# Performance work log

Measured on AMD Instinct MI355X. Metric: run time of the kernel, lower is better.

## Reference

```python
import jax, jax.numpy as jnp
import numpy as np

NUM_HEADS = 8
EPS = 1e-6


def conv1x1(x, w, b):
    # x: [b,c,h,w], w: [out,in], b: [out]  (torch Conv2d 1x1 weight squeezed)
    return jnp.einsum('bchw,oc->bohw', x, w) + b[None, :, None, None]


def feature_map(x):
    return jax.nn.elu(x) + 1.0


def setup_inputs() -> dict:
    key = jax.random.key(0)
    ks = jax.random.split(key, 9)
    C = 512
    s = 1.0 / np.sqrt(C)
    x = jax.random.normal(ks[0], (8, C, 64, 64), dtype=jnp.float32)
    wq = jax.random.normal(ks[1], (C, C), dtype=jnp.float32) * s
    wk = jax.random.normal(ks[2], (C, C), dtype=jnp.float32) * s
    wv = jax.random.normal(ks[3], (C, C), dtype=jnp.float32) * s
    wo = jax.random.normal(ks[4], (C, C), dtype=jnp.float32) * s
    bq = jax.random.normal(ks[5], (C,), dtype=jnp.float32) * 0.01
    bk = jax.random.normal(ks[6], (C,), dtype=jnp.float32) * 0.01
    bv = jax.random.normal(ks[7], (C,), dtype=jnp.float32) * 0.01
    bo = jax.random.normal(ks[8], (C,), dtype=jnp.float32) * 0.01
    return {'x': x, 'wq': wq, 'bq': bq, 'wk': wk, 'bk': bk,
            'wv': wv, 'bv': bv, 'wo': wo, 'bo': bo}


def reference(x, wq, bq, wk, bk, wv, bv, wo, bo):
    b, c, h, w = x.shape
    nh = NUM_HEADS
    hd = c // nh
    L = h * w

    def to_heads(t):
        # [b,c,h,w] -> [b,nh,L,hd]
        return t.reshape(b, nh, hd, L).transpose(0, 1, 3, 2)

    Q = feature_map(to_heads(conv1x1(x, wq, bq)))
    K = feature_map(to_heads(conv1x1(x, wk, bk)))
    V = to_heads(conv1x1(x, wv, bv)) / L  # values / v_length

    KV = jnp.einsum('bhld,bhlv->bhdv', K, V)                 # [b,nh,hd,hd]
    Z = 1.0 / (jnp.einsum('bhld,bhd->bhl', Q, K.sum(axis=-2)) + EPS)
    out = jnp.einsum('bhld,bhdv,bhl->bhlv', Q, KV, Z) * L    # [b,nh,L,hd]

    out = out.transpose(0, 1, 3, 2).reshape(b, c, h, w)
    return conv1x1(out, wo, bo)
```

## Files before the change

### kernel.cpp

```cpp
#include <hip/hip_runtime.h>
#include <hip/hip_bf16.h>
#include <stdint.h>

#define BATCH 8
#define CCH   512
#define NHD   8
#define HD    64
#define LLEN  4096
#define M1    1536

typedef __bf16 bf16x8 __attribute__((ext_vector_type(8)));
typedef __bf16 bf16x4 __attribute__((ext_vector_type(4)));
typedef float  f32x4  __attribute__((ext_vector_type(4)));

__device__ __forceinline__ f32x4 mfma16(bf16x8 a, bf16x8 b, f32x4 c) {
  return __builtin_amdgcn_mfma_f32_16x16x32_bf16(a, b, c, 0, 0, 0);
}

__device__ __forceinline__ void gload_lds16(const void* g, void* l) {
  __builtin_amdgcn_global_load_lds(
      (const __attribute__((address_space(1))) uint32_t*)(uintptr_t)g,
      (__attribute__((address_space(3))) uint32_t*)(uintptr_t)l,
      16, 0, 0);
}

__global__ void pack_w(const float* __restrict__ wq, const float* __restrict__ wk,
                       const float* __restrict__ wv, const float* __restrict__ wo,
                       const float* __restrict__ bq, const float* __restrict__ bk,
                       const float* __restrict__ bv,
                       __bf16* __restrict__ wqkvb, __bf16* __restrict__ wob,
                       float* __restrict__ biasq) {
  const int n = M1 * CCH + CCH * CCH + M1;
  for (int i = blockIdx.x * blockDim.x + threadIdx.x; i < n; i += gridDim.x * blockDim.x) {
    if (i < M1 * CCH) {
      int r = i >> 9, c = i & 511;
      float v = (r < 512) ? wq[r * 512 + c]
              : (r < 1024) ? wk[(r - 512) * 512 + c]
                           : wv[(r - 1024) * 512 + c];
      wqkvb[i] = (__bf16)v;
    } else if (i < M1 * CCH + CCH * CCH) {
      int j = i - M1 * CCH;
      wob[j] = (__bf16)wo[j];
    } else {
      int j = i - M1 * CCH - CCH * CCH;
      biasq[j] = (j < 512) ? bq[j] : (j < 1024) ? bk[j - 512] : bv[j - 1024];
    }
  }
}

__global__ __launch_bounds__(256) void transpose_x(const float* __restrict__ x,
                                                   __bf16* __restrict__ xt) {
  __shared__ float tile[64][65];
  const int b = blockIdx.z, c0 = blockIdx.y * 64, l0 = blockIdx.x * 64;
  const int t = threadIdx.x;
  const int lq = (t & 15) * 4, cr = t >> 4;
  const float* xp = x + ((size_t)b * CCH + c0) * LLEN + l0;
#pragma unroll
  for (int q = 0; q < 4; ++q) {
    const int c = cr + q * 16;
    float4 v = *(const float4*)(xp + (size_t)c * LLEN + lq);
    tile[c][lq + 0] = v.x;
    tile[c][lq + 1] = v.y;
    tile[c][lq + 2] = v.z;
    tile[c][lq + 3] = v.w;
  }
  __syncthreads();
  __bf16* xo = xt + ((size_t)b * LLEN + l0) * CCH + c0;
  const int c4 = (t & 15) * 4, lr = t >> 4;
#pragma unroll
  for (int p = 0; p < 4; ++p) {
    const int l = lr + p * 16;
    bf16x4 o;
#pragma unroll
    for (int i = 0; i < 4; ++i) o[i] = (__bf16)tile[c4 + i][l];
    *(bf16x4*)(xo + (size_t)l * CCH + c4) = o;
  }
}

#define STAGE_A2(tt)                                                         \
  {                                                                          \
    const int bs = ((tt) & 3) * 16384;                                       \
    const int tK = (tt) * 32;                                                \
    gload_lds16(Ag + sOff + tK,         lds + bs + tid * 8);                 \
    gload_lds16(Ag + sOff + 65536 + tK, lds + bs + 4096 + tid * 8);          \
  }
#define STAGE_B2(tt)                                                         \
  {                                                                          \
    const int bs = ((tt) & 3) * 16384;                                       \
    const int tK = (tt) * 32;                                                \
    gload_lds16(Bg + sOff + tK,         lds + bs + 8192 + tid * 8);          \
    gload_lds16(Bg + sOff + 65536 + tK, lds + bs + 12288 + tid * 8);         \
  }

template <int EPI>
__global__ __launch_bounds__(512, 1) void gemm256(
    const __bf16* __restrict__ A, const __bf16* __restrict__ Bm,
    const float* __restrict__ bias,
    __bf16* __restrict__ qt, __bf16* __restrict__ kcm, __bf16* __restrict__ vcm,
    float* __restrict__ out) {
  __shared__ __attribute__((aligned(16))) __bf16 lds[4 * 16384];
  const int b  = blockIdx.z;
  const int n0 = blockIdx.x * 256;
  const int m0 = blockIdx.y * 256;
  const int tid = threadIdx.x;
  const int ll = tid & 63, w = tid >> 6;
  const int wr = w >> 2, wc = w & 3;
  const int lhi = ll >> 4, llo = ll & 15;

  const int Ra = wr * 128 + llo;
  const int aLane = ((Ra >> 1) << 6) + (((((Ra & 1) << 2) | lhi) ^ ((Ra >> 1) & 7)) << 3);
  const int Rb = wc * 64 + llo;
  const int bLane = 8192 + ((Rb >> 1) << 6) + (((((Rb & 1) << 2) | lhi) ^ ((Rb >> 1) & 7)) << 3);

  const int r2s = tid >> 3, c7u = (tid & 7) ^ (r2s & 7);
  const int sRow = (r2s << 1) | (c7u >> 2);
  const int sOff = sRow * CCH + ((c7u & 3) << 3);

  const __bf16* Ag = A + (size_t)m0 * CCH;
  const __bf16* Bg = Bm + ((size_t)b * LLEN + n0) * CCH;

  f32x4 acc[8][4] = {};

  STAGE_A2(0) STAGE_B2(0)
  STAGE_A2(1) STAGE_B2(1)
  asm volatile("s_waitcnt vmcnt(4)" ::: "memory");
  asm volatile("s_barrier" ::: "memory");

  for (int t = 0; t < 16; ++t) {
    const int cb = (t & 3) * 16384;
    bf16x8 af[4], bfr[4];
#pragma unroll
    for (int m = 0; m < 4; ++m) af[m] = *(const bf16x8*)(lds + cb + aLane + m * 512);
#pragma unroll
    for (int n = 0; n < 4; ++n) bfr[n] = *(const bf16x8*)(lds + cb + bLane + n * 512);
    if (t <= 13) STAGE_A2(t + 2)
    asm volatile("s_barrier" ::: "memory");
    asm volatile("s_waitcnt lgkmcnt(0)" ::: "memory");
    __builtin_amdgcn_sched_barrier(0);
    __builtin_amdgcn_s_setprio(1);
#pragma unroll
    for (int m = 0; m < 4; ++m)
#pragma unroll
      for (int n = 0; n < 4; ++n) acc[m][n] = mfma16(af[m], bfr[n], acc[m][n]);
    __builtin_amdgcn_s_setprio(0);
    asm volatile("s_barrier" ::: "memory");
#pragma unroll
    for (int m = 0; m < 4; ++m) af[m] = *(const bf16x8*)(lds + cb + aLane + (m + 4) * 512);
    if (t <= 13) STAGE_B2(t + 2)
    asm volatile("s_barrier" ::: "memory");
    asm volatile("s_waitcnt lgkmcnt(0)" ::: "memory");
    __builtin_amdgcn_sched_barrier(0);
    __builtin_amdgcn_s_setprio(1);
#pragma unroll
    for (int m = 0; m < 4; ++m)
#pragma unroll
      for (int n = 0; n < 4; ++n) acc[m + 4][n] = mfma16(af[m], bfr[n], acc[m + 4][n]);
    __builtin_amdgcn_s_setprio(0);
    if (t < 14)       asm volatile("s_waitcnt vmcnt(4)" ::: "memory");
    else if (t == 14) asm volatile("s_waitcnt vmcnt(0)" ::: "memory");
    asm volatile("s_barrier" ::: "memory");
  }

#pragma unroll
  for (int i = 0; i < 8; ++i) {
    const int o0 = m0 + wr * 128 + i * 16 + lhi * 4;
#pragma unroll
    for (int j = 0; j < 4; ++j) {
      const int col = n0 + wc * 64 + j * 16 + llo;
      if (EPI == 0) {
        if (m0 < 512) {
          bf16x4 pk;
#pragma unroll
          for (int r = 0; r < 4; ++r) {
            float tv = acc[i][j][r] + bias[o0 + r];
            tv = tv > 0.f ? tv + 1.f : __expf(tv);
            pk[r] = (__bf16)tv;
          }
          *(bf16x4*)(qt + ((size_t)b * LLEN + col) * CCH + o0) = pk;
        } else if (m0 < 1024) {
#pragma unroll
          for (int r = 0; r < 4; ++r) {
            float tv = acc[i][j][r] + bias[o0 + r];
            tv = tv > 0.f ? tv + 1.f : __expf(tv);
            kcm[((size_t)b * CCH + (o0 - 512 + r)) * LLEN + col] = (__bf16)tv;
          }
        } else {
#pragma unroll
          for (int r = 0; r < 4; ++r)
            vcm[((size_t)b * CCH + (o0 - 1024 + r)) * LLEN + col] =
                (__bf16)(acc[i][j][r] + bias[o0 + r]);
        }
      } else {
#pragma unroll
        for (int r = 0; r < 4; ++r)
          out[((size_t)b * CCH + o0 + r) * LLEN + col] = acc[i][j][r] + bias[o0 + r];
      }
    }
  }
}

__global__ __launch_bounds__(256) void kv_part_k(const __bf16* __restrict__ kcm,
                                                 const __bf16* __restrict__ vcm,
                                                 float* __restrict__ part,
                                                 float* __restrict__ part_ks) {
  __shared__ float red[8192];
  __shared__ float ksred[4][64];
  const int lc = blockIdx.x, bh = blockIdx.y;
  const int b = bh >> 3, h = bh & 7;
  const int tid = threadIdx.x;
  const int w = tid >> 6, ll = tid & 63, lhi = ll >> 4, llo = ll & 15;
  const __bf16* Kp = kcm + ((size_t)b * CCH + h * 64) * LLEN;
  const __bf16* Vp = vcm + ((size_t)b * CCH + h * 64) * LLEN;
  f32x4 acc[4][4];
#pragma unroll
  for (int i = 0; i < 4; ++i)
#pragma unroll
    for (int j = 0; j < 4; ++j) acc[i][j] = (f32x4){0.f, 0.f, 0.f, 0.f};
  float ks[4] = {0.f, 0.f, 0.f, 0.f};
  const int base = lc * 512 + w * 128 + lhi * 8;
#pragma unroll
  for (int kt = 0; kt < 4; ++kt) {
    const int k0 = base + kt * 32;
    bf16x8 af[4], bfr[4];
#pragma unroll
    for (int i = 0; i < 4; ++i) af[i]  = *(const bf16x8*)(Kp + (size_t)(i * 16 + llo) * LLEN + k0);
#pragma unroll
    for (int i = 0; i < 4; ++i) bfr[i] = *(const bf16x8*)(Vp + (size_t)(i * 16 + llo) * LLEN + k0);
#pragma unroll
    for (int i = 0; i < 4; ++i)
#pragma unroll
      for (int r = 0; r < 8; ++r) ks[i] += (float)af[i][r];
#pragma unroll
    for (int i = 0; i < 4; ++i)
#pragma unroll
      for (int j = 0; j < 4; ++j) acc[i][j] = mfma16(af[i], bfr[j], acc[i][j]);
  }
#pragma unroll
  for (int i = 0; i < 4; ++i) {
    float s = ks[i];
    s += __shfl_xor(s, 16);
    s += __shfl_xor(s, 32);
    if (lhi == 0) ksred[w][i * 16 + llo] = s;
  }
  if (w >= 2) {
#pragma unroll
    for (int i = 0; i < 4; ++i)
#pragma unroll
      for (int j = 0; j < 4; ++j)
        *(f32x4*)(red + (((w - 2) * 16 + i * 4 + j) << 8) + ll * 4) = acc[i][j];
  }
  __syncthreads();
  if (w < 2) {
#pragma unroll
    for (int i = 0; i < 4; ++i)
#pragma unroll
      for (int j = 0; j < 4; ++j)
        acc[i][j] += *(const f32x4*)(red + ((w * 16 + i * 4 + j) << 8) + ll * 4);
  }
  float ksv = 0.f;
  if (w == 1) ksv = ksred[0][ll] + ksred[1][ll] + ksred[2][ll] + ksred[3][ll];
  __syncthreads();
  if (w == 1) {
#pragma unroll
    for (int i = 0; i < 4; ++i)
#pragma unroll
      for (int j = 0; j < 4; ++j)
        *(f32x4*)(red + ((i * 4 + j) << 8) + ll * 4) = acc[i][j];
    part_ks[((size_t)lc * 64 + bh) * 64 + ll] = ksv;
  }
  __syncthreads();
  if (w == 0) {
    float* op = part + ((size_t)lc * 64 + bh) * 4096;
#pragma unroll
    for (int i = 0; i < 4; ++i)
#pragma unroll
      for (int j = 0; j < 4; ++j) {
        acc[i][j] += *(const f32x4*)(red + ((i * 4 + j) << 8) + ll * 4);
#pragma unroll
        for (int r = 0; r < 4; ++r) {
          int d = i * 16 + lhi * 4 + r, v = j * 16 + llo;
          op[d * 64 + v] = acc[i][j][r];
        }
      }
  }
}

__global__ void kv_red_k(const float* __restrict__ part, float* __restrict__ kv) {
  const int i = blockIdx.x * blockDim.x + threadIdx.x;
  float s = 0.f;
#pragma unroll
  for (int lc = 0; lc < 8; ++lc) s += part[(size_t)lc * 262144 + i];
  kv[i] = s;
}

__global__ void ksum_red_k(const float* __restrict__ part_ks, float* __restrict__ ksum) {
  const int i = blockIdx.x * blockDim.x + threadIdx.x;
  float s = 0.f;
#pragma unroll
  for (int lc = 0; lc < 8; ++lc) s += part_ks[(size_t)lc * 4096 + i];
  ksum[i] = s;
}

__global__ __launch_bounds__(256) void apply_k(const __bf16* __restrict__ qt,
                                               const float* __restrict__ kv,
                                               const float* __restrict__ ksum,
                                               __bf16* __restrict__ attn) {
  __shared__ __attribute__((aligned(16))) __bf16 kvT[64 * 68];
  __shared__ float zb[256];
  const int lc = blockIdx.x, bh = blockIdx.y;
  const int b = bh >> 3, h = bh & 7;
  const int tid = threadIdx.x;
  const float* kvp = kv + (size_t)bh * 4096;
  for (int i = tid; i < 4096; i += 256) {
    int d = i >> 6, v = i & 63;
    kvT[v * 68 + d] = (__bf16)kvp[i];
  }
  const int l = lc * 256 + tid;
  const __bf16* qp = qt + ((size_t)b * LLEN + l) * CCH + h * 64;
  const float* ksp = ksum + bh * 64;
  float s = 0.f;
#pragma unroll
  for (int d8 = 0; d8 < 64; d8 += 8) {
    bf16x8 qv = *(const bf16x8*)(qp + d8);
#pragma unroll
    for (int i = 0; i < 8; ++i) s += (float)qv[i] * ksp[d8 + i];
  }
  zb[tid] = 1.0f / (s + 1e-6f);
  __syncthreads();

  const int ll = tid & 63, w = tid >> 6, lhi = ll >> 4, llo = ll & 15;
  f32x4 acc[4][4];
#pragma unroll
  for (int i = 0; i < 4; ++i)
#pragma unroll
    for (int j = 0; j < 4; ++j) acc[i][j] = (f32x4){0.f, 0.f, 0.f, 0.f};
  const __bf16* qbase = qt + ((size_t)b * LLEN + lc * 256 + w * 64) * CCH + h * 64;
#pragma unroll
  for (int kt = 0; kt < 2; ++kt) {
    const int k8 = kt * 32 + lhi * 8;
    bf16x8 af[4], bfr[4];
#pragma unroll
    for (int i = 0; i < 4; ++i)
      af[i] = *(const bf16x8*)(qbase + (size_t)(i * 16 + llo) * CCH + k8);
#pragma unroll
    for (int j = 0; j < 4; ++j) {
      const __bf16* pb = kvT + (j * 16 + llo) * 68 + k8;
      ((bf16x4*)&bfr[j])[0] = *(const bf16x4*)pb;
      ((bf16x4*)&bfr[j])[1] = *(const bf16x4*)(pb + 4);
    }
#pragma unroll
    for (int i = 0; i < 4; ++i)
#pragma unroll
      for (int j = 0; j < 4; ++j) acc[i][j] = mfma16(af[i], bfr[j], acc[i][j]);
  }
  __bf16* ap = attn + ((size_t)b * LLEN + lc * 256) * CCH + h * 64;
#pragma unroll
  for (int i = 0; i < 4; ++i)
#pragma unroll
    for (int j = 0; j < 4; ++j)
#pragma unroll
      for (int r = 0; r < 4; ++r) {
        int ml = w * 64 + i * 16 + lhi * 4 + r;
        int v = j * 16 + llo;
        ap[(size_t)ml * CCH + v] = (__bf16)(acc[i][j][r] * zb[ml]);
      }
}

extern "C" void kernel_launch(void* const* d_in, const int* in_sizes, int n_in,
                              void* d_out, int out_size, void* d_ws, size_t ws_size,
                              hipStream_t stream) {
  const float* x  = (const float*)d_in[0];
  const float* wq = (const float*)d_in[1];
  const float* bq = (const float*)d_in[2];
  const float* wk = (const float*)d_in[3];
  const float* bk = (const float*)d_in[4];
  const float* wv = (const float*)d_in[5];
  const float* bv = (const float*)d_in[6];
  const float* wo = (const float*)d_in[7];
  const float* bo = (const float*)d_in[8];
  float* out = (float*)d_out;

  char* p = (char*)d_ws;
  __bf16* xt    = (__bf16*)p; p += (size_t)BATCH * LLEN * CCH * 2;
  __bf16* qt    = (__bf16*)p; p += (size_t)BATCH * LLEN * CCH * 2;
  __bf16* kcm   = (__bf16*)p; p += (size_t)BATCH * CCH * LLEN * 2;
  __bf16* vcm   = (__bf16*)p; p += (size_t)BATCH * CCH * LLEN * 2;
  __bf16* wqkvb = (__bf16*)p; p += (size_t)M1 * CCH * 2;
  __bf16* wob   = (__bf16*)p; p += (size_t)CCH * CCH * 2;
  float*  biasq = (float*)p;  p += (size_t)M1 * 4;
  float*  ksum  = (float*)p;  p += (size_t)BATCH * CCH * 4;
  float*  part  = (float*)p;  p += (size_t)8 * 64 * HD * HD * 4;
  float*  kvb   = (float*)p;  p += (size_t)64 * HD * HD * 4;
  float*  pks   = (float*)p;  p += (size_t)8 * 64 * 64 * 4;
  __bf16* attn  = xt;

  pack_w<<<1024, 256, 0, stream>>>(wq, wk, wv, wo, bq, bk, bv, wqkvb, wob, biasq);
  transpose_x<<<dim3(64, 8, BATCH), 256, 0, stream>>>(x, xt);
  gemm256<0><<<dim3(16, 6, BATCH), 512, 0, stream>>>(wqkvb, xt, biasq, qt, kcm, vcm, nullptr);
  kv_part_k<<<dim3(8, 64), 256, 0, stream>>>(kcm, vcm, part, pks);
  kv_red_k<<<1024, 256, 0, stream>>>(part, kvb);
  ksum_red_k<<<16, 256, 0, stream>>>(pks, ksum);
  apply_k<<<dim3(16, 64), 256, 0, stream>>>(qt, kvb, ksum, attn);
  gemm256<1><<<dim3(16, 2, BATCH), 512, 0, stream>>>(wob, attn, bo, nullptr, nullptr, nullptr, out);
}
```

Before: 176.1 us.

## Fold KV matrix into output projection weights and rework GEMM LDS layout

Replaces the per-token Q·KV apply kernel with a per-batch fold of Wo and KV into a combined weight, so the output GEMM consumes normalized Q directly. Q is scaled in place by the Z normalizer in a lightweight kernel. The GEMM's LDS swizzle and fragment loading are also reorganized, with a three-stage prefetch depth and loads of all eight A fragments per k-step. This is meant to remove the apply pass over Q and attention writes, at the cost of a per-batch 512x512 weight and batched A operands in the second GEMM.

```diff
diff --git a/kernel.cpp b/kernel.cpp
--- a/kernel.cpp
+++ b/kernel.cpp
@@ -25,12 +25,11 @@
 }
 
 __global__ void pack_w(const float* __restrict__ wq, const float* __restrict__ wk,
-                       const float* __restrict__ wv, const float* __restrict__ wo,
+                       const float* __restrict__ wv,
                        const float* __restrict__ bq, const float* __restrict__ bk,
                        const float* __restrict__ bv,
-                       __bf16* __restrict__ wqkvb, __bf16* __restrict__ wob,
-                       float* __restrict__ biasq) {
-  const int n = M1 * CCH + CCH * CCH + M1;
+                       __bf16* __restrict__ wqkvb, float* __restrict__ biasq) {
+  const int n = M1 * CCH + M1;
   for (int i = blockIdx.x * blockDim.x + threadIdx.x; i < n; i += gridDim.x * blockDim.x) {
     if (i < M1 * CCH) {
       int r = i >> 9, c = i & 511;
@@ -38,11 +37,8 @@
               : (r < 1024) ? wk[(r - 512) * 512 + c]
                            : wv[(r - 1024) * 512 + c];
       wqkvb[i] = (__bf16)v;
-    } else if (i < M1 * CCH + CCH * CCH) {
+    } else {
       int j = i - M1 * CCH;
-      wob[j] = (__bf16)wo[j];
-    } else {
-      int j = i - M1 * CCH - CCH * CCH;
       biasq[j] = (j < 512) ? bq[j] : (j < 1024) ? bk[j - 512] : bv[j - 1024];
     }
   }
@@ -77,19 +73,19 @@
   }
 }
 
-#define STAGE_A2(tt)                                                         \
-  {                                                                          \
-    const int bs = ((tt) & 3) * 16384;                                       \
-    const int tK = (tt) * 32;                                                \
-    gload_lds16(Ag + sOff + tK,         lds + bs + tid * 8);                 \
-    gload_lds16(Ag + sOff + 65536 + tK, lds + bs + 4096 + tid * 8);          \
-  }
-#define STAGE_B2(tt)                                                         \
-  {                                                                          \
-    const int bs = ((tt) & 3) * 16384;                                       \
-    const int tK = (tt) * 32;                                                \
-    gload_lds16(Bg + sOff + tK,         lds + bs + 8192 + tid * 8);          \
-    gload_lds16(Bg + sOff + 65536 + tK, lds + bs + 12288 + tid * 8);         \
+#define STAGE_A(tt)                                                           \
+  {                                                                           \
+    const int dbase = ((tt) & 3) * 16384;                                     \
+    const int tK = (tt) * 32;                                                 \
+    gload_lds16(Ag + srcOff + tK,         lds + dbase + tid * 8);             \
+    gload_lds16(Ag + srcOff + tK + 65536, lds + dbase + 4096 + tid * 8);      \
+  }
+#define STAGE_B(tt)                                                           \
+  {                                                                           \
+    const int dbase = ((tt) & 3) * 16384 + 8192;                              \
+    const int tK = (tt) * 32;                                                 \
+    gload_lds16(Bg + srcOff + tK,         lds + dbase + tid * 8);             \
+    gload_lds16(Bg + srcOff + tK + 65536, lds + dbase + 4096 + tid * 8);      \
   }
 
 template <int EPI>
@@ -107,58 +103,62 @@
   const int wr = w >> 2, wc = w & 3;
   const int lhi = ll >> 4, llo = ll & 15;
 
-  const int Ra = wr * 128 + llo;
-  const int aLane = ((Ra >> 1) << 6) + (((((Ra & 1) << 2) | lhi) ^ ((Ra >> 1) & 7)) << 3);
-  const int Rb = wc * 64 + llo;
-  const int bLane = 8192 + ((Rb >> 1) << 6) + (((((Rb & 1) << 2) | lhi) ^ ((Rb >> 1) & 7)) << 3);
-
-  const int r2s = tid >> 3, c7u = (tid & 7) ^ (r2s & 7);
-  const int sRow = (r2s << 1) | (c7u >> 2);
-  const int sOff = sRow * CCH + ((c7u & 3) << 3);
-
-  const __bf16* Ag = A + (size_t)m0 * CCH;
+  const int slotE = ((lhi ^ ((llo >> 1) & 3)) << 3);
+  int aOff[8], bOff[4];
+#pragma unroll
+  for (int m = 0; m < 8; ++m) aOff[m] = (wr * 128 + m * 16 + llo) * 32 + slotE;
+#pragma unroll
+  for (int n = 0; n < 4; ++n) bOff[n] = 8192 + (wc * 64 + n * 16 + llo) * 32 + slotE;
+
+  const int sRow = tid >> 2;
+  const int srcOff = sRow * CCH + ((((tid & 3) ^ ((sRow >> 1) & 3))) << 3);
+
+  const __bf16* Ag = (EPI == 0 ? A + (size_t)m0 * CCH
+                               : A + (size_t)b * CCH * CCH + (size_t)m0 * CCH);
   const __bf16* Bg = Bm + ((size_t)b * LLEN + n0) * CCH;
 
   f32x4 acc[8][4] = {};
 
-  STAGE_A2(0) STAGE_B2(0)
-  STAGE_A2(1) STAGE_B2(1)
-  asm volatile("s_waitcnt vmcnt(4)" ::: "memory");
-  asm volatile("s_barrier" ::: "memory");
+  STAGE_A(0) STAGE_B(0) STAGE_A(1) STAGE_B(1) STAGE_A(2) STAGE_B(2)
+  asm volatile("s_waitcnt vmcnt(8)" ::: "memory");
+  __builtin_amdgcn_s_barrier();
 
   for (int t = 0; t < 16; ++t) {
     const int cb = (t & 3) * 16384;
-    bf16x8 af[4], bfr[4];
-#pragma unroll
-    for (int m = 0; m < 4; ++m) af[m] = *(const bf16x8*)(lds + cb + aLane + m * 512);
-#pragma unroll
-    for (int n = 0; n < 4; ++n) bfr[n] = *(const bf16x8*)(lds + cb + bLane + n * 512);
-    if (t <= 13) STAGE_A2(t + 2)
-    asm volatile("s_barrier" ::: "memory");
+    bf16x8 aq[8], bq[4];
+#pragma unroll
+    for (int m = 0; m < 8; ++m) aq[m] = *(const bf16x8*)(lds + cb + aOff[m]);
+    bq[0] = *(const bf16x8*)(lds + cb + bOff[0]);
+    bq[1] = *(const bf16x8*)(lds + cb + bOff[1]);
+    if (t <= 12) STAGE_A(t + 3)
+    __builtin_amdgcn_s_barrier();
     asm volatile("s_waitcnt lgkmcnt(0)" ::: "memory");
     __builtin_amdgcn_sched_barrier(0);
     __builtin_amdgcn_s_setprio(1);
 #pragma unroll
-    for (int m = 0; m < 4; ++m)
-#pragma unroll
-      for (int n = 0; n < 4; ++n) acc[m][n] = mfma16(af[m], bfr[n], acc[m][n]);
+    for (int m = 0; m < 8; ++m) {
+      acc[m][0] = mfma16(aq[m], bq[0], acc[m][0]);
+      acc[m][1] = mfma16(aq[m], bq[1], acc[m][1]);
+    }
     __builtin_amdgcn_s_setprio(0);
-    asm volatile("s_barrier" ::: "memory");
-#pragma unroll
-    for (int m = 0; m < 4; ++m) af[m] = *(const bf16x8*)(lds + cb + aLane + (m + 4) * 512);
-    if (t <= 13) STAGE_B2(t + 2)
-    asm volatile("s_barrier" ::: "memory");
+    __builtin_amdgcn_s_barrier();
+    bq[2] = *(const bf16x8*)(lds + cb + bOff[2]);
+    bq[3] = *(const bf16x8*)(lds + cb + bOff[3]);
+    if (t <= 12) STAGE_B(t + 3)
+    if (t <= 12)      asm volatile("s_waitcnt vmcnt(8)" ::: "memory");
+    else if (t == 13) asm volatile("s_waitcnt vmcnt(4)" ::: "memory");
+    else if (t == 14) asm volatile("s_waitcnt vmcnt(0)" ::: "memory");
+    __builtin_amdgcn_s_barrier();
     asm volatile("s_waitcnt lgkmcnt(0)" ::: "memory");
     __builtin_amdgcn_sched_barrier(0);
     __builtin_amdgcn_s_setprio(1);
 #pragma unroll
-    for (int m = 0; m < 4; ++m)
-#pragma unroll
-      for (int n = 0; n < 4; ++n) acc[m + 4][n] = mfma16(af[m], bfr[n], acc[m + 4][n]);
+    for (int m = 0; m < 8; ++m) {
+      acc[m][2] = mfma16(aq[m], bq[2], acc[m][2]);
+      acc[m][3] = mfma16(aq[m], bq[3], acc[m][3]);
+    }
     __builtin_amdgcn_s_setprio(0);
-    if (t < 14)       asm volatile("s_waitcnt vmcnt(4)" ::: "memory");
-    else if (t == 14) asm volatile("s_waitcnt vmcnt(0)" ::: "memory");
-    asm volatile("s_barrier" ::: "memory");
+    __builtin_amdgcn_s_barrier();
   }
 
 #pragma unroll
@@ -301,69 +301,74 @@
   ksum[i] = s;
 }
 
-__global__ __launch_bounds__(256) void apply_k(const __bf16* __restrict__ qt,
-                                               const float* __restrict__ kv,
-                                               const float* __restrict__ ksum,
-                                               __bf16* __restrict__ attn) {
-  __shared__ __attribute__((aligned(16))) __bf16 kvT[64 * 68];
-  __shared__ float zb[256];
-  const int lc = blockIdx.x, bh = blockIdx.y;
-  const int b = bh >> 3, h = bh & 7;
+__global__ __launch_bounds__(256) void fold_k(const float* __restrict__ wo,
+                                              const float* __restrict__ kvb,
+                                              __bf16* __restrict__ wokv) {
+  const int h = blockIdx.x, b = blockIdx.y;
   const int tid = threadIdx.x;
-  const float* kvp = kv + (size_t)bh * 4096;
-  for (int i = tid; i < 4096; i += 256) {
-    int d = i >> 6, v = i & 63;
-    kvT[v * 68 + d] = (__bf16)kvp[i];
-  }
-  const int l = lc * 256 + tid;
-  const __bf16* qp = qt + ((size_t)b * LLEN + l) * CCH + h * 64;
-  const float* ksp = ksum + bh * 64;
-  float s = 0.f;
-#pragma unroll
-  for (int d8 = 0; d8 < 64; d8 += 8) {
-    bf16x8 qv = *(const bf16x8*)(qp + d8);
-#pragma unroll
-    for (int i = 0; i < 8; ++i) s += (float)qv[i] * ksp[d8 + i];
-  }
-  zb[tid] = 1.0f / (s + 1e-6f);
+  const int w = tid >> 6, ll = tid & 63, lhi = ll >> 4, llo = ll & 15;
+  const float* kvp = kvb + (size_t)(b * 8 + h) * 4096;
+  f32x4 acc[8][4] = {};
+#pragma unroll
+  for (int ks = 0; ks < 2; ++ks) {
+    bf16x8 bfr[4];
+#pragma unroll
+    for (int n = 0; n < 4; ++n) {
+      const float* p = kvp + (n * 16 + llo) * 64 + ks * 32 + lhi * 8;
+      bf16x8 v;
+#pragma unroll
+      for (int e = 0; e < 8; ++e) v[e] = (__bf16)p[e];
+      bfr[n] = v;
+    }
+#pragma unroll
+    for (int m = 0; m < 8; ++m) {
+      const float* p = wo + (size_t)(w * 128 + m * 16 + llo) * 512 + h * 64 + ks * 32 + lhi * 8;
+      bf16x8 av;
+#pragma unroll
+      for (int e = 0; e < 8; ++e) av[e] = (__bf16)p[e];
+#pragma unroll
+      for (int n = 0; n < 4; ++n) acc[m][n] = mfma16(av, bfr[n], acc[m][n]);
+    }
+  }
+#pragma unroll
+  for (int m = 0; m < 8; ++m)
+#pragma unroll
+    for (int n = 0; n < 4; ++n)
+#pragma unroll
+      for (int r = 0; r < 4; ++r) {
+        int o = w * 128 + m * 16 + lhi * 4 + r;
+        int d = n * 16 + llo;
+        wokv[((size_t)b * 512 + o) * 512 + h * 64 + d] = (__bf16)acc[m][n][r];
+      }
+}
+
+__global__ __launch_bounds__(256) void zscale_k(__bf16* __restrict__ qt,
+                                                const float* __restrict__ ksumf) {
+  __shared__ float ks[512];
+  const int b = blockIdx.y;
+  const int l0 = blockIdx.x * 32;
+  const int tid = threadIdx.x;
+  ks[tid]       = ksumf[b * 512 + tid];
+  ks[tid + 256] = ksumf[b * 512 + tid + 256];
   __syncthreads();
-
-  const int ll = tid & 63, w = tid >> 6, lhi = ll >> 4, llo = ll & 15;
-  f32x4 acc[4][4];
-#pragma unroll
-  for (int i = 0; i < 4; ++i)
-#pragma unroll
-    for (int j = 0; j < 4; ++j) acc[i][j] = (f32x4){0.f, 0.f, 0.f, 0.f};
-  const __bf16* qbase = qt + ((size_t)b * LLEN + lc * 256 + w * 64) * CCH + h * 64;
-#pragma unroll
-  for (int kt = 0; kt < 2; ++kt) {
-    const int k8 = kt * 32 + lhi * 8;
-    bf16x8 af[4], bfr[4];
-#pragma unroll
-    for (int i = 0; i < 4; ++i)
-      af[i] = *(const bf16x8*)(qbase + (size_t)(i * 16 + llo) * CCH + k8);
-#pragma unroll
-    for (int j = 0; j < 4; ++j) {
-      const __bf16* pb = kvT + (j * 16 + llo) * 68 + k8;
-      ((bf16x4*)&bfr[j])[0] = *(const bf16x4*)pb;
-      ((bf16x4*)&bfr[j])[1] = *(const bf16x4*)(pb + 4);
-    }
-#pragma unroll
-    for (int i = 0; i < 4; ++i)
-#pragma unroll
-      for (int j = 0; j < 4; ++j) acc[i][j] = mfma16(af[i], bfr[j], acc[i][j]);
-  }
-  __bf16* ap = attn + ((size_t)b * LLEN + lc * 256) * CCH + h * 64;
-#pragma unroll
-  for (int i = 0; i < 4; ++i)
-#pragma unroll
-    for (int j = 0; j < 4; ++j)
-#pragma unroll
-      for (int r = 0; r < 4; ++r) {
-        int ml = w * 64 + i * 16 + lhi * 4 + r;
-        int v = j * 16 + llo;
-        ap[(size_t)ml * CCH + v] = (__bf16)(acc[i][j][r] * zb[ml]);
-      }
+  const int r = tid >> 3, h = tid & 7;
+  __bf16* qp = qt + ((size_t)b * LLEN + l0 + r) * CCH + h * 64;
+  bf16x8 v[8];
+  float dot = 0.f;
+#pragma unroll
+  for (int e = 0; e < 8; ++e) {
+    v[e] = *(const bf16x8*)(qp + e * 8);
+#pragma unroll
+    for (int i = 0; i < 8; ++i) dot += (float)v[e][i] * ks[h * 64 + e * 8 + i];
+  }
+  const float z = 1.0f / (dot + 1e-6f);
+#pragma unroll
+  for (int e = 0; e < 8; ++e) {
+    bf16x8 o;
+#pragma unroll
+    for (int i = 0; i < 8; ++i) o[i] = (__bf16)((float)v[e][i] * z);
+    *(bf16x8*)(qp + e * 8) = o;
+  }
 }
 
 extern "C" void kernel_launch(void* const* d_in, const int* in_sizes, int n_in,
@@ -386,20 +391,20 @@
   __bf16* kcm   = (__bf16*)p; p += (size_t)BATCH * CCH * LLEN * 2;
   __bf16* vcm   = (__bf16*)p; p += (size_t)BATCH * CCH * LLEN * 2;
   __bf16* wqkvb = (__bf16*)p; p += (size_t)M1 * CCH * 2;
-  __bf16* wob   = (__bf16*)p; p += (size_t)CCH * CCH * 2;
   float*  biasq = (float*)p;  p += (size_t)M1 * 4;
-  float*  ksum  = (float*)p;  p += (size_t)BATCH * CCH * 4;
+  float*  ksumf = (float*)p;  p += (size_t)BATCH * CCH * 4;
   float*  part  = (float*)p;  p += (size_t)8 * 64 * HD * HD * 4;
   float*  kvb   = (float*)p;  p += (size_t)64 * HD * HD * 4;
   float*  pks   = (float*)p;  p += (size_t)8 * 64 * 64 * 4;
-  __bf16* attn  = xt;
-
-  pack_w<<<1024, 256, 0, stream>>>(wq, wk, wv, wo, bq, bk, bv, wqkvb, wob, biasq);
+  __bf16* wokv  = (__bf16*)p; p += (size_t)BATCH * CCH * CCH * 2;
+
+  pack_w<<<1024, 256, 0, stream>>>(wq, wk, wv, bq, bk, bv, wqkvb, biasq);
   transpose_x<<<dim3(64, 8, BATCH), 256, 0, stream>>>(x, xt);
   gemm256<0><<<dim3(16, 6, BATCH), 512, 0, stream>>>(wqkvb, xt, biasq, qt, kcm, vcm, nullptr);
   kv_part_k<<<dim3(8, 64), 256, 0, stream>>>(kcm, vcm, part, pks);
   kv_red_k<<<1024, 256, 0, stream>>>(part, kvb);
-  ksum_red_k<<<16, 256, 0, stream>>>(pks, ksum);
-  apply_k<<<dim3(16, 64), 256, 0, stream>>>(qt, kvb, ksum, attn);
-  gemm256<1><<<dim3(16, 2, BATCH), 512, 0, stream>>>(wob, attn, bo, nullptr, nullptr, nullptr, out);
-}
+  ksum_red_k<<<16, 256, 0, stream>>>(pks, ksumf);
+  fold_k<<<dim3(8, 8), 256, 0, stream>>>(wo, kvb, wokv);
+  zscale_k<<<dim3(128, BATCH), 256, 0, stream>>>(qt, ksumf);
+  gemm256<1><<<dim3(16, 2, BATCH), 512, 0, stream>>>(wokv, qt, bo, nullptr, nullptr, vcm, out);
+}
```

Result: slower. 187.7 us (+6.6%).

## Replace 256x256 GEMM with 128x128 double-buffered tiles and LDS-staged coalesced epilogues

Applied to the files above, without the earlier changes.

The 256x256 single-block-per-CU GEMM with a 4-stage LDS pipeline becomes a 128x128 tile kernel with 256 threads, a 2-stage double buffer and up to 4 blocks per CU. This gives more blocks in flight and lower LDS use per block, but each block reuses less data from each load. The epilogues now stage results through LDS so that global writes of Q, K, V and the fp32 output are wide coalesced vector stores instead of scattered scalar ones. The transpose kernel also widens its bf16 stores from 4 to 8 elements.

```diff
diff --git a/kernel.cpp b/kernel.cpp
--- a/kernel.cpp
+++ b/kernel.cpp
@@ -66,135 +66,152 @@
   }
   __syncthreads();
   __bf16* xo = xt + ((size_t)b * LLEN + l0) * CCH + c0;
-  const int c4 = (t & 15) * 4, lr = t >> 4;
-#pragma unroll
-  for (int p = 0; p < 4; ++p) {
-    const int l = lr + p * 16;
-    bf16x4 o;
-#pragma unroll
-    for (int i = 0; i < 4; ++i) o[i] = (__bf16)tile[c4 + i][l];
-    *(bf16x4*)(xo + (size_t)l * CCH + c4) = o;
-  }
-}
-
-#define STAGE_A2(tt)                                                         \
+  const int c8 = (t & 7) * 8, lr = t >> 3;
+#pragma unroll
+  for (int p = 0; p < 2; ++p) {
+    const int l = lr + p * 32;
+    bf16x8 o;
+#pragma unroll
+    for (int i = 0; i < 8; ++i) o[i] = (__bf16)tile[c8 + i][l];
+    *(bf16x8*)(xo + (size_t)l * CCH + c8) = o;
+  }
+}
+
+#define STG128(tt, buf)                                                      \
   {                                                                          \
-    const int bs = ((tt) & 3) * 16384;                                       \
-    const int tK = (tt) * 32;                                                \
-    gload_lds16(Ag + sOff + tK,         lds + bs + tid * 8);                 \
-    gload_lds16(Ag + sOff + 65536 + tK, lds + bs + 4096 + tid * 8);          \
-  }
-#define STAGE_B2(tt)                                                         \
-  {                                                                          \
-    const int bs = ((tt) & 3) * 16384;                                       \
-    const int tK = (tt) * 32;                                                \
-    gload_lds16(Bg + sOff + tK,         lds + bs + 8192 + tid * 8);          \
-    gload_lds16(Bg + sOff + 65536 + tK, lds + bs + 12288 + tid * 8);         \
+    const __bf16* As_ = Ag + (tt) * 32;                                      \
+    const __bf16* Bs_ = Bg + (tt) * 32;                                      \
+    __bf16* dA = lds + (buf) * 8192;                                         \
+    __bf16* dB = dA + 4096;                                                  \
+    gload_lds16(As_ + srcOff1, dA + tid * 8);                                \
+    gload_lds16(As_ + srcOff2, dA + tid * 8 + 2048);                         \
+    gload_lds16(Bs_ + srcOff1, dB + tid * 8);                                \
+    gload_lds16(Bs_ + srcOff2, dB + tid * 8 + 2048);                         \
   }
 
 template <int EPI>
-__global__ __launch_bounds__(512, 1) void gemm256(
+__global__ __launch_bounds__(256, 4) void gemm128(
     const __bf16* __restrict__ A, const __bf16* __restrict__ Bm,
     const float* __restrict__ bias,
     __bf16* __restrict__ qt, __bf16* __restrict__ kcm, __bf16* __restrict__ vcm,
     float* __restrict__ out) {
-  __shared__ __attribute__((aligned(16))) __bf16 lds[4 * 16384];
+  __shared__ __attribute__((aligned(16))) __bf16 lds[17408];
   const int b  = blockIdx.z;
-  const int n0 = blockIdx.x * 256;
-  const int m0 = blockIdx.y * 256;
+  const int n0 = blockIdx.x * 128;
+  const int m0 = blockIdx.y * 128;
   const int tid = threadIdx.x;
   const int ll = tid & 63, w = tid >> 6;
-  const int wr = w >> 2, wc = w & 3;
+  const int wr = w >> 1, wc = w & 1;
   const int lhi = ll >> 4, llo = ll & 15;
 
-  const int Ra = wr * 128 + llo;
-  const int aLane = ((Ra >> 1) << 6) + (((((Ra & 1) << 2) | lhi) ^ ((Ra >> 1) & 7)) << 3);
-  const int Rb = wc * 64 + llo;
-  const int bLane = 8192 + ((Rb >> 1) << 6) + (((((Rb & 1) << 2) | lhi) ^ ((Rb >> 1) & 7)) << 3);
-
-  const int r2s = tid >> 3, c7u = (tid & 7) ^ (r2s & 7);
-  const int sRow = (r2s << 1) | (c7u >> 2);
-  const int sOff = sRow * CCH + ((c7u & 3) << 3);
+  const int slotE = ((lhi ^ ((llo >> 1) & 3)) << 3);
+  int aOff[4], bOff[4];
+#pragma unroll
+  for (int m = 0; m < 4; ++m) aOff[m] = (wr * 64 + m * 16 + llo) * 32 + slotE;
+#pragma unroll
+  for (int n = 0; n < 4; ++n) bOff[n] = 4096 + (wc * 64 + n * 16 + llo) * 32 + slotE;
+
+  const int s1 = tid, s2 = tid + 256;
+  const int r1 = s1 >> 2, r2s = s2 >> 2;
+  const int srcOff1 = r1 * CCH + (((s1 & 3) ^ ((r1 >> 1) & 3)) << 3);
+  const int srcOff2 = r2s * CCH + (((s2 & 3) ^ ((r2s >> 1) & 3)) << 3);
 
   const __bf16* Ag = A + (size_t)m0 * CCH;
   const __bf16* Bg = Bm + ((size_t)b * LLEN + n0) * CCH;
 
-  f32x4 acc[8][4] = {};
-
-  STAGE_A2(0) STAGE_B2(0)
-  STAGE_A2(1) STAGE_B2(1)
-  asm volatile("s_waitcnt vmcnt(4)" ::: "memory");
-  asm volatile("s_barrier" ::: "memory");
+  f32x4 acc[4][4] = {};
+
+  STG128(0, 0)
+  __syncthreads();
 
   for (int t = 0; t < 16; ++t) {
-    const int cb = (t & 3) * 16384;
+    const int buf = t & 1;
+    if (t < 15) STG128(t + 1, buf ^ 1)
     bf16x8 af[4], bfr[4];
-#pragma unroll
-    for (int m = 0; m < 4; ++m) af[m] = *(const bf16x8*)(lds + cb + aLane + m * 512);
-#pragma unroll
-    for (int n = 0; n < 4; ++n) bfr[n] = *(const bf16x8*)(lds + cb + bLane + n * 512);
-    if (t <= 13) STAGE_A2(t + 2)
-    asm volatile("s_barrier" ::: "memory");
-    asm volatile("s_waitcnt lgkmcnt(0)" ::: "memory");
-    __builtin_amdgcn_sched_barrier(0);
-    __builtin_amdgcn_s_setprio(1);
+    const __bf16* base = lds + buf * 8192;
+#pragma unroll
+    for (int m = 0; m < 4; ++m) af[m] = *(const bf16x8*)(base + aOff[m]);
+#pragma unroll
+    for (int n = 0; n < 4; ++n) bfr[n] = *(const bf16x8*)(base + bOff[n]);
 #pragma unroll
     for (int m = 0; m < 4; ++m)
 #pragma unroll
       for (int n = 0; n < 4; ++n) acc[m][n] = mfma16(af[m], bfr[n], acc[m][n]);
-    __builtin_amdgcn_s_setprio(0);
-    asm volatile("s_barrier" ::: "memory");
-#pragma unroll
-    for (int m = 0; m < 4; ++m) af[m] = *(const bf16x8*)(lds + cb + aLane + (m + 4) * 512);
-    if (t <= 13) STAGE_B2(t + 2)
-    asm volatile("s_barrier" ::: "memory");
-    asm volatile("s_waitcnt lgkmcnt(0)" ::: "memory");
-    __builtin_amdgcn_sched_barrier(0);
-    __builtin_amdgcn_s_setprio(1);
-#pragma unroll
-    for (int m = 0; m < 4; ++m)
-#pragma unroll
-      for (int n = 0; n < 4; ++n) acc[m + 4][n] = mfma16(af[m], bfr[n], acc[m + 4][n]);
-    __builtin_amdgcn_s_setprio(0);
-    if (t < 14)       asm volatile("s_waitcnt vmcnt(4)" ::: "memory");
-    else if (t == 14) asm volatile("s_waitcnt vmcnt(0)" ::: "memory");
-    asm volatile("s_barrier" ::: "memory");
-  }
-
-#pragma unroll
-  for (int i = 0; i < 8; ++i) {
-    const int o0 = m0 + wr * 128 + i * 16 + lhi * 4;
-#pragma unroll
-    for (int j = 0; j < 4; ++j) {
-      const int col = n0 + wc * 64 + j * 16 + llo;
-      if (EPI == 0) {
-        if (m0 < 512) {
+    __syncthreads();
+  }
+
+  if (EPI == 0) {
+    if (m0 < 512) {
+#pragma unroll
+      for (int i = 0; i < 4; ++i)
+#pragma unroll
+        for (int j = 0; j < 4; ++j) {
+          const int chq = wr * 64 + i * 16 + lhi * 4;
+          const int lq  = wc * 64 + j * 16 + llo;
           bf16x4 pk;
 #pragma unroll
           for (int r = 0; r < 4; ++r) {
-            float tv = acc[i][j][r] + bias[o0 + r];
+            float tv = acc[i][j][r] + bias[m0 + chq + r];
             tv = tv > 0.f ? tv + 1.f : __expf(tv);
             pk[r] = (__bf16)tv;
           }
-          *(bf16x4*)(qt + ((size_t)b * LLEN + col) * CCH + o0) = pk;
-        } else if (m0 < 1024) {
+          *(bf16x4*)(lds + lq * 136 + chq) = pk;
+        }
+      __syncthreads();
+      const int l = tid >> 1, seg = tid & 1;
+      __bf16* dst = qt + ((size_t)b * LLEN + n0 + l) * CCH + m0 + seg * 64;
+      const __bf16* src = lds + l * 136 + seg * 64;
+#pragma unroll
+      for (int k = 0; k < 8; ++k)
+        *(bf16x8*)(dst + k * 8) = *(const bf16x8*)(src + k * 8);
+    } else {
+      const bool isK = (m0 < 1024);
+      __bf16* base_out = isK ? kcm + ((size_t)b * CCH + (m0 - 512)) * LLEN
+                             : vcm + ((size_t)b * CCH + (m0 - 1024)) * LLEN;
+#pragma unroll
+      for (int i = 0; i < 4; ++i)
+#pragma unroll
+        for (int j = 0; j < 4; ++j) {
+          const int chq = wr * 64 + i * 16 + lhi * 4;
+          const int lq  = wc * 64 + j * 16 + llo;
 #pragma unroll
           for (int r = 0; r < 4; ++r) {
-            float tv = acc[i][j][r] + bias[o0 + r];
-            tv = tv > 0.f ? tv + 1.f : __expf(tv);
-            kcm[((size_t)b * CCH + (o0 - 512 + r)) * LLEN + col] = (__bf16)tv;
+            float tv = acc[i][j][r] + bias[m0 + chq + r];
+            if (isK) tv = tv > 0.f ? tv + 1.f : __expf(tv);
+            lds[(chq + r) * 136 + lq] = (__bf16)tv;
           }
-        } else {
+        }
+      __syncthreads();
+      const int ch = tid >> 1, seg = tid & 1;
+      __bf16* dst = base_out + (size_t)ch * LLEN + n0 + seg * 64;
+      const __bf16* src = lds + ch * 136 + seg * 64;
+#pragma unroll
+      for (int k = 0; k < 8; ++k)
+        *(bf16x8*)(dst + k * 8) = *(const bf16x8*)(src + k * 8);
+    }
+  } else {
+    float* flds = (float*)lds;
+#pragma unroll
+    for (int p = 0; p < 2; ++p) {
+      if (p) __syncthreads();
+#pragma unroll
+      for (int i = 0; i < 4; ++i)
+#pragma unroll
+        for (int jj = 0; jj < 2; ++jj) {
+          const int j = p * 2 + jj;
+          const int chq = wr * 64 + i * 16 + lhi * 4;
+          const int cc  = wc * 32 + jj * 16 + llo;
 #pragma unroll
           for (int r = 0; r < 4; ++r)
-            vcm[((size_t)b * CCH + (o0 - 1024 + r)) * LLEN + col] =
-                (__bf16)(acc[i][j][r] + bias[o0 + r]);
+            flds[(chq + r) * 68 + cc] = acc[i][j][r] + bias[m0 + chq + r];
         }
-      } else {
-#pragma unroll
-        for (int r = 0; r < 4; ++r)
-          out[((size_t)b * CCH + o0 + r) * LLEN + col] = acc[i][j][r] + bias[o0 + r];
-      }
+      __syncthreads();
+      const int ch = tid >> 1, half = tid & 1;
+      float* dst = out + ((size_t)b * CCH + m0 + ch) * LLEN + n0 + half * 64 + p * 32;
+      const float* src = flds + ch * 68 + half * 32;
+#pragma unroll
+      for (int k = 0; k < 8; ++k)
+        *(float4*)(dst + k * 4) = *(const float4*)(src + k * 4);
     }
   }
 }
@@ -396,10 +413,11 @@
 
   pack_w<<<1024, 256, 0, stream>>>(wq, wk, wv, wo, bq, bk, bv, wqkvb, wob, biasq);
   transpose_x<<<dim3(64, 8, BATCH), 256, 0, stream>>>(x, xt);
-  gemm256<0><<<dim3(16, 6, BATCH), 512, 0, stream>>>(wqkvb, xt, biasq, qt, kcm, vcm, nullptr);
+  gemm128<0><<<dim3(32, 12, BATCH), 256, 0, stream>>>(wqkvb, xt, biasq, qt, kcm, vcm, nullptr);
   kv_part_k<<<dim3(8, 64), 256, 0, stream>>>(kcm, vcm, part, pks);
   kv_red_k<<<1024, 256, 0, stream>>>(part, kvb);
   ksum_red_k<<<16, 256, 0, stream>>>(pks, ksum);
   apply_k<<<dim3(16, 64), 256, 0, stream>>>(qt, kvb, ksum, attn);
-  gemm256<1><<<dim3(16, 2, BATCH), 512, 0, stream>>>(wob, attn, bo, nullptr, nullptr, nullptr, out);
-}
+  gemm128<1><<<dim3(32, 4, BATCH), 256, 0, stream>>>(wob, attn, bo, nullptr, nullptr,
+                                                     nullptr, out);
+}
```

New measurement: 190.7 us. +8.3%, slower.
